# Kernel optimization log

Measured on AMD Instinct MI355X. Metric: run time of the kernel, lower is better.

## Reference

```python
import jax, jax.numpy as jnp
import numpy as np

DIM = 1024
HEADS = 16
B, N = 4, 1024

def setup_inputs() -> dict:
    key = jax.random.key(0)
    k1, k2, k3 = jax.random.split(key, 3)
    x = jax.random.normal(k1, (B, N, DIM), dtype=jnp.float32)
    # xavier-uniform-ish init scale
    Wqkv = jax.random.normal(k2, (3 * DIM, DIM), dtype=jnp.float32) * (1.0 / np.sqrt(DIM))
    bqkv = jnp.zeros((3 * DIM,), dtype=jnp.float32)
    W1 = jax.random.normal(k3, (DIM, DIM), dtype=jnp.float32) * (1.0 / np.sqrt(DIM))
    b1 = jnp.zeros((DIM,), dtype=jnp.float32)
    return {"x": x, "Wqkv": Wqkv, "bqkv": bqkv, "W1": W1, "b1": b1}

def reference(x, Wqkv, bqkv, W1, b1):
    b, n, dim = x.shape
    h = HEADS
    d = dim // h
    scale = dim ** (-0.5)  # NOTE: module scales by full dim, not head dim
    qkv = x @ Wqkv.T + bqkv  # [b, n, 3*dim]
    qkv = qkv.reshape(b, n, 3, h, d)
    q = jnp.transpose(qkv[:, :, 0], (0, 2, 1, 3))  # [b, h, n, d]
    k = jnp.transpose(qkv[:, :, 1], (0, 2, 1, 3))
    v = jnp.transpose(qkv[:, :, 2], (0, 2, 1, 3))
    dots = jnp.einsum('bhid,bhjd->bhij', q, k) * scale
    attn = jax.nn.softmax(dots, axis=-1)
    out = jnp.einsum('bhij,bhjd->bhid', attn, v)
    out = jnp.transpose(out, (0, 2, 1, 3)).reshape(b, n, dim)
    out = out @ W1.T + b1
    return out
```

## Files before the change

### kernel.cpp

```cpp
#include <hip/hip_runtime.h>
#include <cmath>

typedef __bf16 bf16;
typedef __bf16 bf16x8 __attribute__((ext_vector_type(8)));
typedef __bf16 bf16x4 __attribute__((ext_vector_type(4)));
typedef float f32x4 __attribute__((ext_vector_type(4)));

#define MFMA16(a, b, c) __builtin_amdgcn_mfma_f32_16x16x32_bf16(a, b, c, 0, 0, 0)

__device__ __forceinline__ void load_lds16(const void* g, void* l) {
    __builtin_amdgcn_global_load_lds(
        (const __attribute__((address_space(1))) void*)g,
        (__attribute__((address_space(3))) void*)l, 16, 0, 0);
}

__device__ __forceinline__ bf16x8 load8(const bf16* p) { return *(const bf16x8*)p; }
__device__ __forceinline__ bf16x8 load8(const float* p) {
    float4 f0 = *(const float4*)p;
    float4 f1 = *(const float4*)(p + 4);
    bf16x8 r;
    r[0] = (bf16)f0.x; r[1] = (bf16)f0.y; r[2] = (bf16)f0.z; r[3] = (bf16)f0.w;
    r[4] = (bf16)f1.x; r[5] = (bf16)f1.y; r[6] = (bf16)f1.z; r[7] = (bf16)f1.w;
    return r;
}

__global__ __launch_bounds__(256) void cvt3(
    const float* __restrict__ s0, bf16* __restrict__ d0, int n0,
    const float* __restrict__ s1, bf16* __restrict__ d1, int n1,
    const float* __restrict__ s2, bf16* __restrict__ d2, int n2)
{
    int i = blockIdx.x * 256 + threadIdx.x;
    const float* s; bf16* d; int base;
    if (i < n0)                { s = s0; d = d0; base = i; }
    else if (i < n0 + n1)      { s = s1; d = d1; base = i - n0; }
    else if (i < n0 + n1 + n2) { s = s2; d = d2; base = i - n0 - n1; }
    else return;
    *(bf16x8*)(d + (size_t)base * 8) = load8(s + (size_t)base * 8);
}

template <int EPI, typename TB, int BN>
__global__ __launch_bounds__(256) void gemm_bt(
    const bf16* __restrict__ A, const TB* __restrict__ Bm,
    const float* __restrict__ bias,
    bf16* __restrict__ qo, bf16* __restrict__ ko, bf16* __restrict__ vto,
    float* __restrict__ C, int M, int N, int K)
{
    constexpr int WN = BN / 2;
    constexpr int JN = WN / 16;
    constexpr int SLOTS = (128 + BN) * 8;

    __shared__ bf16 As[128 * 64];
    __shared__ bf16 Bs[BN * 64];

    const int tid = threadIdx.x;
    const int l   = tid & 63;
    const int w   = tid >> 6;
    const int wm  = w & 1, wn = w >> 1;
    const int l15 = l & 15;
    const int g   = l >> 4;
    const int swz = l15 & 7;
    const int m0  = blockIdx.y * 128;
    const int n0  = blockIdx.x * BN;

    f32x4 acc[4][JN] = {};

    for (int k0 = 0; k0 < K; k0 += 64) {
        __syncthreads();
        #pragma unroll
        for (int it = 0; it < SLOTS / 256; ++it) {
            int s = it * 256 + w * 64 + l;
            if (s < 1024) {
                int row = s >> 3, pc = s & 7;
                int lc  = pc ^ (row & 7);
                load_lds16(A + (size_t)(m0 + row) * K + k0 + lc * 8, &As[s * 8]);
            } else {
                int t = s - 1024;
                int row = t >> 3, pc = t & 7;
                int lc  = pc ^ (row & 7);
                if constexpr (sizeof(TB) == 2) {
                    load_lds16(Bm + (size_t)(n0 + row) * K + k0 + lc * 8, &Bs[t * 8]);
                } else {
                    *(bf16x8*)&Bs[t * 8] = load8(Bm + (size_t)(n0 + row) * K + k0 + lc * 8);
                }
            }
        }
        __syncthreads();
        #pragma unroll
        for (int kk = 0; kk < 64; kk += 32) {
            bf16x8 aF[4], bF[JN];
            #pragma unroll
            for (int i = 0; i < 4; ++i)
                aF[i] = *(const bf16x8*)&As[(wm * 64 + i * 16 + l15) * 64
                                            + ((((kk >> 3) + g) ^ swz) * 8)];
            #pragma unroll
            for (int j = 0; j < JN; ++j)
                bF[j] = *(const bf16x8*)&Bs[(wn * WN + j * 16 + l15) * 64
                                            + ((((kk >> 3) + g) ^ swz) * 8)];
            #pragma unroll
            for (int i = 0; i < 4; ++i)
                #pragma unroll
                for (int j = 0; j < JN; ++j)
                    acc[i][j] = MFMA16(aF[i], bF[j], acc[i][j]);
        }
    }

    #pragma unroll
    for (int j = 0; j < JN; ++j) {
        int gcol = n0 + wn * WN + j * 16 + l15;
        float bv = bias[gcol];
        if (EPI == 0) {
            int which = gcol >> 10;
            int h  = (gcol >> 6) & 15;
            int dd = gcol & 63;
            #pragma unroll
            for (int i = 0; i < 4; ++i) {
                #pragma unroll
                for (int r = 0; r < 4; ++r) {
                    int grow = m0 + wm * 64 + i * 16 + g * 4 + r;
                    int b    = grow >> 10;
                    int npos = grow & 1023;
                    float v  = acc[i][j][r] + bv;
                    size_t bh = (size_t)(b * 16 + h);
                    if (which == 0)
                        qo[(bh * 1024 + npos) * 64 + dd] = (bf16)v;
                    else if (which == 1)
                        ko[(bh * 1024 + npos) * 64 + dd] = (bf16)v;
                    else
                        vto[(bh * 64 + dd) * 1024 + npos] = (bf16)v;
                }
            }
        } else {
            #pragma unroll
            for (int i = 0; i < 4; ++i)
                #pragma unroll
                for (int r = 0; r < 4; ++r) {
                    int grow = m0 + wm * 64 + i * 16 + g * 4 + r;
                    C[(size_t)grow * N + gcol] = acc[i][j][r] + bv;
                }
        }
    }
}

__global__ __launch_bounds__(256) void attn_fused(
    const bf16* __restrict__ qb, const bf16* __restrict__ kb,
    const bf16* __restrict__ vtb, bf16* __restrict__ attn)
{
    __shared__ bf16 Ks[2][64 * 64];
    __shared__ bf16 Vts[2][64 * 64];
    __shared__ bf16 Ps[4][16][40];

    const int tid = threadIdx.x;
    const int l   = tid & 63;
    const int w   = tid >> 6;
    const int l15 = l & 15;
    const int g   = l >> 4;
    const int swz = l15 & 7;
    const int bid = blockIdx.x;
    const int bh  = bid & 63;
    const int qc  = bid >> 6;
    const int m0  = qc * 64;

    const bf16* q_bh  = qb  + (size_t)bh * 65536;
    const bf16* k_bh  = kb  + (size_t)bh * 65536;
    const bf16* vt_bh = vtb + (size_t)bh * 65536;

    bf16x8 qf[2];
    #pragma unroll
    for (int kk = 0; kk < 2; ++kk)
        qf[kk] = *(const bf16x8*)(q_bh + (size_t)(m0 + w * 16 + l15) * 64
                                  + kk * 32 + g * 8);

    f32x4 o[4] = {};
    float lsum = 0.f;

    const float C_EXP = 0.04508422f;

    auto stage = [&](int buf, int j0) {
        #pragma unroll
        for (int it = 0; it < 2; ++it) {
            int s   = it * 256 + w * 64 + l;
            int row = s >> 3, pc = s & 7;
            int lc  = pc ^ (row & 7);
            load_lds16(k_bh + (size_t)(j0 + row) * 64 + lc * 8, &Ks[buf][s * 8]);
            load_lds16(vt_bh + (size_t)row * 1024 + j0 + lc * 8, &Vts[buf][s * 8]);
        }
    };

    stage(0, 0);

    for (int t = 0; t < 16; ++t) {
        const int c = t & 1;
        __syncthreads();
        if (t < 15) stage(c ^ 1, (t + 1) * 64);

        f32x4 s4[4] = {};
        #pragma unroll
        for (int kk = 0; kk < 2; ++kk) {
            bf16x8 kf[4];
            #pragma unroll
            for (int js = 0; js < 4; ++js)
                kf[js] = *(const bf16x8*)&Ks[c][(js * 16 + l15) * 64
                                                + (((kk * 4 + g) ^ swz) * 8)];
            __builtin_amdgcn_s_setprio(1);
            #pragma unroll
            for (int js = 0; js < 4; ++js)
                s4[js] = MFMA16(kf[js], qf[kk], s4[js]);
            __builtin_amdgcn_s_setprio(0);
        }

        #pragma unroll
        for (int h = 0; h < 2; ++h) {
            #pragma unroll
            for (int jsl = 0; jsl < 2; ++jsl) {
                int js = h * 2 + jsl;
                bf16x4 pk;
                float ps = 0.f;
                #pragma unroll
                for (int r = 0; r < 4; ++r) {
                    float p = exp2f(s4[js][r] * C_EXP);
                    ps += p;
                    pk[r] = (bf16)p;
                }
                lsum += ps;
                *(bf16x4*)&Ps[w][l15][jsl * 16 + g * 4] = pk;
            }
            bf16x8 vf[4];
            #pragma unroll
            for (int ns = 0; ns < 4; ++ns)
                vf[ns] = *(const bf16x8*)&Vts[c][(ns * 16 + l15) * 64
                                                 + (((h * 4 + g) ^ swz) * 8)];
            bf16x8 pf = *(const bf16x8*)&Ps[w][l15][g * 8];
            __builtin_amdgcn_s_setprio(1);
            #pragma unroll
            for (int ns = 0; ns < 4; ++ns)
                o[ns] = MFMA16(pf, vf[ns], o[ns]);
            __builtin_amdgcn_s_setprio(0);
        }
    }

    float t = lsum;
    t += __shfl_xor(t, 16);
    t += __shfl_xor(t, 32);

    #pragma unroll
    for (int r = 0; r < 4; ++r) {
        float inv = 1.0f / __shfl(t, g * 4 + r);
        int grow = m0 + w * 16 + g * 4 + r;
        size_t obase = ((size_t)(bh >> 4) * 1024 + grow) * 1024 + (bh & 15) * 64;
        #pragma unroll
        for (int ns = 0; ns < 4; ++ns)
            attn[obase + ns * 16 + l15] = (bf16)(o[ns][r] * inv);
    }
}

extern "C" void kernel_launch(void* const* d_in, const int* in_sizes, int n_in,
                              void* d_out, int out_size, void* d_ws, size_t ws_size,
                              hipStream_t stream)
{
    const float* x    = (const float*)d_in[0];
    const float* Wqkv = (const float*)d_in[1];
    const float* bqkv = (const float*)d_in[2];
    const float* W1   = (const float*)d_in[3];
    const float* b1   = (const float*)d_in[4];
    float* out = (float*)d_out;

    const size_t SEG = (size_t)4 * 16 * 1024 * 64;
    bf16* xbf  = (bf16*)d_ws;
    bf16* qb   = xbf + SEG;
    bf16* kb   = qb + SEG;
    bf16* vtb  = kb + SEG;
    bf16* attnb = xbf;
    bf16* wqkvbf = vtb + SEG;
    bf16* w1bf   = wqkvbf + 3145728;

    const bool cw = ws_size >= (size_t)(5 * SEG) * sizeof(bf16);

    const int nx = 524288;
    const int nw = cw ? 393216 : 0;
    const int n1 = cw ? 131072 : 0;
    const int tot = nx + nw + n1;
    cvt3<<<dim3((tot + 255) / 256), 256, 0, stream>>>(
        x, xbf, nx, Wqkv, wqkvbf, nw, W1, w1bf, n1);

    if (cw)
        gemm_bt<0, bf16, 128><<<dim3(24, 32), 256, 0, stream>>>(
            xbf, wqkvbf, bqkv, qb, kb, vtb, nullptr, 4096, 3072, 1024);
    else
        gemm_bt<0, float, 128><<<dim3(24, 32), 256, 0, stream>>>(
            xbf, Wqkv, bqkv, qb, kb, vtb, nullptr, 4096, 3072, 1024);

    attn_fused<<<dim3(1024), 256, 0, stream>>>(qb, kb, vtb, attnb);

    if (cw)
        gemm_bt<1, bf16, 64><<<dim3(16, 32), 256, 0, stream>>>(
            attnb, w1bf, b1, nullptr, nullptr, nullptr, out, 4096, 1024, 1024);
    else
        gemm_bt<1, float, 64><<<dim3(16, 32), 256, 0, stream>>>(
            attnb, W1, b1, nullptr, nullptr, nullptr, out, 4096, 1024, 1024);
}
```

Baseline: 171.7 us.

## Process two query groups per warp in attention to reuse K/V tiles

Each warp in the attention kernel now handles 32 query rows (two 16-row groups) instead of 16, so each block covers 128 queries and the grid is halved. Every K and V fragment loaded from LDS and every staged tile is reused across twice as many MFMAs, which cuts LDS traffic and global K/V restaging per unit of work. The cost is more accumulator registers, which may lower occupancy, and only 512 blocks, which may underfill the GPU's compute units.

```diff
diff --git a/kernel.cpp b/kernel.cpp
--- a/kernel.cpp
+++ b/kernel.cpp
@@ -147,7 +147,7 @@
 {
     __shared__ bf16 Ks[2][64 * 64];
     __shared__ bf16 Vts[2][64 * 64];
-    __shared__ bf16 Ps[4][16][40];
+    __shared__ bf16 Ps[4][2][16][40];
 
     const int tid = threadIdx.x;
     const int l   = tid & 63;
@@ -158,20 +158,22 @@
     const int bid = blockIdx.x;
     const int bh  = bid & 63;
     const int qc  = bid >> 6;
-    const int m0  = qc * 64;
+    const int m0  = qc * 128;
 
     const bf16* q_bh  = qb  + (size_t)bh * 65536;
     const bf16* k_bh  = kb  + (size_t)bh * 65536;
     const bf16* vt_bh = vtb + (size_t)bh * 65536;
 
-    bf16x8 qf[2];
+    bf16x8 qf[2][2];
     #pragma unroll
-    for (int kk = 0; kk < 2; ++kk)
-        qf[kk] = *(const bf16x8*)(q_bh + (size_t)(m0 + w * 16 + l15) * 64
-                                  + kk * 32 + g * 8);
-
-    f32x4 o[4] = {};
-    float lsum = 0.f;
+    for (int qg = 0; qg < 2; ++qg)
+        #pragma unroll
+        for (int kk = 0; kk < 2; ++kk)
+            qf[qg][kk] = *(const bf16x8*)(q_bh
+                + (size_t)(m0 + w * 32 + qg * 16 + l15) * 64 + kk * 32 + g * 8);
+
+    f32x4 o[2][4] = {};
+    float lsum[2] = {0.f, 0.f};
 
     const float C_EXP = 0.04508422f;
 
@@ -193,7 +195,7 @@
         __syncthreads();
         if (t < 15) stage(c ^ 1, (t + 1) * 64);
 
-        f32x4 s4[4] = {};
+        f32x4 s4[2][4] = {};
         #pragma unroll
         for (int kk = 0; kk < 2; ++kk) {
             bf16x8 kf[4];
@@ -203,53 +205,69 @@
                                                 + (((kk * 4 + g) ^ swz) * 8)];
             __builtin_amdgcn_s_setprio(1);
             #pragma unroll
-            for (int js = 0; js < 4; ++js)
-                s4[js] = MFMA16(kf[js], qf[kk], s4[js]);
+            for (int qg = 0; qg < 2; ++qg)
+                #pragma unroll
+                for (int js = 0; js < 4; ++js)
+                    s4[qg][js] = MFMA16(kf[js], qf[qg][kk], s4[qg][js]);
             __builtin_amdgcn_s_setprio(0);
         }
 
         #pragma unroll
         for (int h = 0; h < 2; ++h) {
             #pragma unroll
-            for (int jsl = 0; jsl < 2; ++jsl) {
-                int js = h * 2 + jsl;
-                bf16x4 pk;
-                float ps = 0.f;
-                #pragma unroll
-                for (int r = 0; r < 4; ++r) {
-                    float p = exp2f(s4[js][r] * C_EXP);
-                    ps += p;
-                    pk[r] = (bf16)p;
+            for (int qg = 0; qg < 2; ++qg) {
+                #pragma unroll
+                for (int jsl = 0; jsl < 2; ++jsl) {
+                    int js = h * 2 + jsl;
+                    bf16x4 pk;
+                    float ps = 0.f;
+                    #pragma unroll
+                    for (int r = 0; r < 4; ++r) {
+                        float p = exp2f(s4[qg][js][r] * C_EXP);
+                        ps += p;
+                        pk[r] = (bf16)p;
+                    }
+                    lsum[qg] += ps;
+                    *(bf16x4*)&Ps[w][qg][l15][jsl * 16 + g * 4] = pk;
                 }
-                lsum += ps;
-                *(bf16x4*)&Ps[w][l15][jsl * 16 + g * 4] = pk;
             }
             bf16x8 vf[4];
             #pragma unroll
             for (int ns = 0; ns < 4; ++ns)
                 vf[ns] = *(const bf16x8*)&Vts[c][(ns * 16 + l15) * 64
                                                  + (((h * 4 + g) ^ swz) * 8)];
-            bf16x8 pf = *(const bf16x8*)&Ps[w][l15][g * 8];
             __builtin_amdgcn_s_setprio(1);
             #pragma unroll
+            for (int qg = 0; qg < 2; ++qg) {
+                bf16x8 pf = *(const bf16x8*)&Ps[w][qg][l15][g * 8];
+                #pragma unroll
+                for (int ns = 0; ns < 4; ++ns)
+                    o[qg][ns] = MFMA16(pf, vf[ns], o[qg][ns]);
+            }
+            __builtin_amdgcn_s_setprio(0);
+        }
+    }
+
+    float tden[2];
+    #pragma unroll
+    for (int qg = 0; qg < 2; ++qg) {
+        float t = lsum[qg];
+        t += __shfl_xor(t, 16);
+        t += __shfl_xor(t, 32);
+        tden[qg] = t;
+    }
+
+    #pragma unroll
+    for (int qg = 0; qg < 2; ++qg) {
+        #pragma unroll
+        for (int r = 0; r < 4; ++r) {
+            float inv = 1.0f / __shfl(tden[qg], g * 4 + r);
+            int grow = m0 + w * 32 + qg * 16 + g * 4 + r;
+            size_t obase = ((size_t)(bh >> 4) * 1024 + grow) * 1024 + (bh & 15) * 64;
+            #pragma unroll
             for (int ns = 0; ns < 4; ++ns)
-                o[ns] = MFMA16(pf, vf[ns], o[ns]);
-            __builtin_amdgcn_s_setprio(0);
-        }
-    }
-
-    float t = lsum;
-    t += __shfl_xor(t, 16);
-    t += __shfl_xor(t, 32);
-
-    #pragma unroll
-    for (int r = 0; r < 4; ++r) {
-        float inv = 1.0f / __shfl(t, g * 4 + r);
-        int grow = m0 + w * 16 + g * 4 + r;
-        size_t obase = ((size_t)(bh >> 4) * 1024 + grow) * 1024 + (bh & 15) * 64;
-        #pragma unroll
-        for (int ns = 0; ns < 4; ++ns)
-            attn[obase + ns * 16 + l15] = (bf16)(o[ns][r] * inv);
+                attn[obase + ns * 16 + l15] = (bf16)(o[qg][ns][r] * inv);
+        }
     }
 }
 
@@ -289,7 +307,7 @@
         gemm_bt<0, float, 128><<<dim3(24, 32), 256, 0, stream>>>(
             xbf, Wqkv, bqkv, qb, kb, vtb, nullptr, 4096, 3072, 1024);
 
-    attn_fused<<<dim3(1024), 256, 0, stream>>>(qb, kb, vtb, attnb);
+    attn_fused<<<dim3(512), 256, 0, stream>>>(qb, kb, vtb, attnb);
 
     if (cw)
         gemm_bt<1, bf16, 64><<<dim3(16, 32), 256, 0, stream>>>(
```

Measured after the change: 173.6 us. No clear change (+1.1%).
